# Kernel optimization log

Hardware: AMD Instinct MI355X
Metric: run time of the kernel (lower is better)

## Reference

```python
import jax, jax.numpy as jnp
import numpy as np

B, S, D, H, T, MAXLEN = 8, 1024, 768, 12, 384, 1024
HD = D // H  # spatial head dim = 64
SCALE = HD ** -0.5


def setup_inputs() -> dict:
    key = jax.random.key(0)
    ks = jax.random.split(key, 16)

    def lin(k, din, dout):
        kw, _ = jax.random.split(k)
        w = jax.random.normal(kw, (din, dout), jnp.float32) / np.sqrt(din).astype(np.float32)
        b = jnp.zeros((dout,), jnp.float32)
        return w, b

    Wqs, bqs = lin(ks[0], D, D)
    Wks, bks = lin(ks[1], D, D)
    Wvs, bvs = lin(ks[2], D, D)
    Wqt, bqt = lin(ks[3], T, D)
    Wkt, bkt = lin(ks[4], T, D)
    Wvt, bvt = lin(ks[5], T, D)
    Er = jax.random.normal(ks[6], (MAXLEN, HD), jnp.float32)
    patches = jax.random.normal(ks[7], (B, S, D), jnp.float32)
    time_emb = jax.random.normal(ks[8], (B, T), jnp.float32)
    return dict(patches=patches, time_emb=time_emb,
                Wqs=Wqs, bqs=bqs, Wks=Wks, bks=bks, Wvs=Wvs, bvs=bvs,
                Wqt=Wqt, bqt=bqt, Wkt=Wkt, bkt=bkt, Wvt=Wvt, bvt=bvt, Er=Er)


def _skew(QEr):
    # QEr: [B, H, S, S] -> pad one zero col on the left, reshape, drop first row.
    b, h, r, c = QEr.shape
    padded = jnp.pad(QEr, ((0, 0), (0, 0), (0, 0), (1, 0)))  # [B,H,r,c+1]
    reshaped = padded.reshape(b, h, c + 1, r)
    return reshaped[:, :, 1:, :]  # [B,H,S,S]


def reference(patches, time_emb, Wqs, bqs, Wks, bks, Wvs, bvs,
              Wqt, bqt, Wkt, bkt, Wvt, bvt, Er):
    b, s, _ = patches.shape

    def heads(x):  # [B,S,D] -> [B,H,S,HD]
        return x.reshape(b, -1, H, HD).transpose(0, 2, 1, 3)

    qs = heads(patches @ Wqs + bqs)
    ks = heads(patches @ Wks + bks)
    vs = heads(patches @ Wvs + bvs)
    qt = heads(time_emb @ Wqt + bqt)  # [B,H,1,HD]
    kt = heads(time_emb @ Wkt + bkt)
    vt = heads(time_emb @ Wvt + bvt)

    q = qs + qt
    k = ks + kt
    v = vs + vt

    Er_slice = Er[MAXLEN - s:, :]                      # [S, HD]
    QEr = jnp.einsum('bhsd,td->bhst', qs, Er_slice)    # [B,H,S,S]
    Srel = _skew(QEr)

    scores = (jnp.einsum('bhqd,bhkd->bhqk', q, k) + Srel) * SCALE
    attn = jax.nn.softmax(scores, axis=-1)
    out = jnp.einsum('bhqk,bhkd->bhqd', attn, v)       # [B,H,S,HD]
    return out.transpose(0, 2, 1, 3).reshape(b, s, H * HD)
```

## Files before the change

### kernel.cpp

```cpp
#include <hip/hip_runtime.h>

typedef __attribute__((ext_vector_type(8))) short short8;
typedef __attribute__((ext_vector_type(4))) float floatx4;

#define CSC 0.1803368801f

__device__ __forceinline__ unsigned short f2b(float f){
  unsigned int u = __builtin_bit_cast(unsigned int, f);
  unsigned int r = (u + 0x7fffu + ((u >> 16) & 1u)) >> 16;
  return (unsigned short)r;
}
__device__ __forceinline__ float b2f(unsigned short h){
  unsigned int u = ((unsigned int)h) << 16;
  return __builtin_bit_cast(float, u);
}
__device__ __forceinline__ floatx4 mfma16(short8 a, short8 b, floatx4 c){
  return __builtin_amdgcn_mfma_f32_16x16x32_bf16(a, b, c, 0, 0, 0);
}
__device__ __forceinline__ void gload_lds16(const unsigned short* g, unsigned short* l){
  __builtin_amdgcn_global_load_lds(
      (const __attribute__((address_space(1))) unsigned int*)g,
      (__attribute__((address_space(3))) unsigned int*)l, 16, 0, 0);
}

__global__ __launch_bounds__(256) void prep_kernel(
    const float* __restrict__ patches, const float* __restrict__ Er,
    const float* __restrict__ temb,
    const float* __restrict__ Wqt, const float* __restrict__ bqt,
    const float* __restrict__ Wkt, const float* __restrict__ bkt,
    const float* __restrict__ Wvt, const float* __restrict__ bvt,
    const float* __restrict__ Wqs, const float* __restrict__ Wks,
    const float* __restrict__ Wvs,
    unsigned short* __restrict__ Pb, unsigned short* __restrict__ Erb,
    float* __restrict__ Tmat, unsigned short* __restrict__ Wb){
  int blk = blockIdx.x, tid = threadIdx.x;
  if (blk < 3104){
    const float* src; unsigned short* dst; int idx;
    if (blk < 3072){ idx = blk*2048 + tid*8; src = patches; dst = Pb; }
    else           { idx = (blk-3072)*2048 + tid*8; src = Er; dst = Erb; }
    float4 f0 = *(const float4*)(src + idx);
    float4 f1 = *(const float4*)(src + idx + 4);
    uint4 pk;
    pk.x = (unsigned)f2b(f0.x) | ((unsigned)f2b(f0.y)<<16);
    pk.y = (unsigned)f2b(f0.z) | ((unsigned)f2b(f0.w)<<16);
    pk.z = (unsigned)f2b(f1.x) | ((unsigned)f2b(f1.y)<<16);
    pk.w = (unsigned)f2b(f1.z) | ((unsigned)f2b(f1.w)<<16);
    *(uint4*)(dst + idx) = pk;
  } else if (blk < 3248){
    int idx = blk - 3104;
    int g = idx / 48, rem = idx % 48, bb = rem / 6, kc = rem % 6;
    const float* Wt = (g==0)? Wqt : (g==1)? Wkt : Wvt;
    const float* bt = (g==0)? bqt : (g==1)? bkt : bvt;
    __shared__ float emb[64];
    if (tid < 64) emb[tid] = temb[bb*384 + kc*64 + tid];
    __syncthreads();
    float a0 = 0.f, a1 = 0.f, a2 = 0.f;
    #pragma unroll 8
    for (int t=0;t<64;t++){
      float e = emb[t];
      const float* wr = Wt + (kc*64 + t)*768;
      a0 += e*wr[tid]; a1 += e*wr[tid+256]; a2 += e*wr[tid+512];
    }
    if (kc == 0){ a0 += bt[tid]; a1 += bt[tid+256]; a2 += bt[tid+512]; }
    float s = (g==0) ? CSC : 1.0f;
    float* dst = Tmat + g*6144 + bb*768;
    atomicAdd(&dst[tid],     a0*s);
    atomicAdd(&dst[tid+256], a1*s);
    atomicAdd(&dst[tid+512], a2*s);
  } else {
    int tb = blk - 3248;
    int g = tb / 144, rem = tb % 144;
    int by = rem / 12, bx = rem % 12;
    __shared__ float tile[64][65];
    const float* W = (g==0) ? Wqs : (g==1) ? Wks : Wvs;
    int r0 = by*64, c0 = bx*64;
    int tx = tid & 63, ty = tid >> 6;
    #pragma unroll
    for (int i=0;i<16;i++){
      int r = i*4 + ty;
      tile[r][tx] = W[(r0+r)*768 + c0 + tx];
    }
    __syncthreads();
    unsigned short* dst = Wb + g*589824;
    #pragma unroll
    for (int i=0;i<16;i++){
      int rr = i*4 + ty;
      dst[(c0+rr)*768 + r0 + tx] = f2b(tile[tx][rr]);
    }
  }
}

__global__ __launch_bounds__(256, 3) void qkv_gemm(
    const unsigned short* __restrict__ Pb, const unsigned short* __restrict__ Wb,
    const float* __restrict__ bq, const float* __restrict__ bk,
    const float* __restrict__ bv, const float* __restrict__ Tmat,
    unsigned short* __restrict__ Qs, unsigned short* __restrict__ K,
    unsigned short* __restrict__ V){
  __shared__ unsigned short smem_q[26112];
  unsigned short* a_lds = smem_q;
  unsigned short* b_lds = smem_q + 8192;
  int g = blockIdx.z;
  int m0 = blockIdx.x*128, n0 = blockIdx.y*192;
  int tid = threadIdx.x, w = tid>>6, lane = tid&63, quad = lane>>4, l16 = lane&15;
  int wr = w>>1, wc = w&1;
  const unsigned short* Wg = Wb + g*589824;
  const float* bias = (g==0)? bq : (g==1)? bk : bv;
  floatx4 acc[4][6];
  #pragma unroll
  for (int i=0;i<4;i++)
    #pragma unroll
    for (int j=0;j<6;j++) acc[i][j] = (floatx4){0.f,0.f,0.f,0.f};

  int rsub = lane>>3;
  int csw  = (((lane&7) ^ rsub) << 3);
  int sw   = l16 & 7;

  for (int kt=0; kt<12; kt++){
    int k0 = kt*64;
    __syncthreads();
    #pragma unroll
    for (int j=0;j<4;j++){
      int chunk = w*4 + j;
      int r = chunk*8 + rsub;
      gload_lds16(&Pb[(m0+r)*768 + k0 + csw], &a_lds[chunk*512]);
    }
    #pragma unroll
    for (int j=0;j<6;j++){
      int chunk = w*6 + j;
      int r = chunk*8 + rsub;
      gload_lds16(&Wg[(n0+r)*768 + k0 + csw], &b_lds[chunk*512]);
    }
    __syncthreads();
    #pragma unroll
    for (int ks=0; ks<2; ks++){
      short8 af[4], bf[6];
      int cc = ((ks*4 + quad) ^ sw) << 3;
      #pragma unroll
      for (int mb=0;mb<4;mb++)
        af[mb] = *(const short8*)&a_lds[(wr*64+mb*16+l16)*64 + cc];
      #pragma unroll
      for (int nb=0;nb<6;nb++)
        bf[nb] = *(const short8*)&b_lds[(wc*96+nb*16+l16)*64 + cc];
      #pragma unroll
      for (int mb=0;mb<4;mb++)
        #pragma unroll
        for (int nb=0;nb<6;nb++)
          acc[mb][nb] = mfma16(af[mb], bf[nb], acc[mb][nb]);
    }
  }
  if (g < 2){
    #pragma unroll
    for (int mb=0;mb<4;mb++)
    #pragma unroll
    for (int nb=0;nb<6;nb++)
    #pragma unroll
    for (int reg=0;reg<4;reg++){
      int m = m0 + wr*64 + mb*16 + quad*4 + reg;
      int n = n0 + wc*96 + nb*16 + l16;
      int bb = m >> 10, s = m & 1023, h = n >> 6, hd = n & 63;
      float v = acc[mb][nb][reg] + bias[n];
      int base = (bb*12 + h) << 16;
      if (g == 0){
        Qs[base + (s<<6) + hd] = f2b(v * CSC);
      } else {
        float tadd = Tmat[6144 + bb*768 + n];
        K[base + (s<<6) + hd] = f2b(v + tadd);
      }
    }
  } else {
    __syncthreads();
    int bb = m0 >> 10;
    #pragma unroll
    for (int mb=0;mb<4;mb++)
    #pragma unroll
    for (int nb=0;nb<6;nb++)
    #pragma unroll
    for (int reg=0;reg<4;reg++){
      int ml = wr*64 + mb*16 + quad*4 + reg;
      int nl = wc*96 + nb*16 + l16;
      int n = n0 + nl;
      float v = acc[mb][nb][reg] + bias[n] + Tmat[12288 + bb*768 + n];
      smem_q[nl*136 + ml] = f2b(v);
    }
    __syncthreads();
    int s0 = m0 & 1023;
    #pragma unroll
    for (int i=0;i<12;i++){
      int idx = i*256 + tid;
      int r = idx >> 4, c8 = (idx & 15) << 3;
      int n = n0 + r, h = n >> 6, hd = n & 63;
      int base = (bb*12 + h) << 16;
      *(uint4*)&V[base + (hd<<10) + s0 + c8] = *(const uint4*)&smem_q[r*136 + c8];
    }
  }
}

__global__ __launch_bounds__(256, 3) void attn_kernel(
    const unsigned short* __restrict__ Qsp, const unsigned short* __restrict__ Kp,
    const unsigned short* __restrict__ Vtp, const unsigned short* __restrict__ Erb,
    const float* __restrict__ Tq, float* __restrict__ out){
  __shared__ __align__(16) char smem[29696];
  unsigned short* k_lds  = (unsigned short*)smem;
  unsigned short* v_lds  = (unsigned short*)(smem + 9216);
  unsigned short* pw_all = (unsigned short*)(smem + 18432);

  int tid = threadIdx.x, w = tid>>6, lane = tid&63, quad = lane>>4, l16 = lane&15;
  unsigned short* pw = pw_all + w*1408;
  int wg = blockIdx.x;
  int b = wg & 7, slot = wg >> 3;
  int h = slot >> 3, q0 = (slot & 7) << 7;
  int hb = (b*12 + h) << 16;
  const unsigned short* Qsh = Qsp + hb;
  const unsigned short* Kh  = Kp  + hb;
  const unsigned short* Vh  = Vtp + hb;
  const float* tqv = Tq + b*768 + h*64;

  int frow = w*16 + l16;
  short8 qf[2][2], qlo[2][2], qhi[2][2];
  #pragma unroll
  for (int sub=0; sub<2; sub++){
    int qrow = q0 + sub*64 + frow;
    int qrow1 = (qrow < 1023) ? qrow+1 : 1023;
    #pragma unroll
    for (int ks=0; ks<2; ks++){
      int c = ks*32 + quad*8;
      qlo[sub][ks] = *(const short8*)&Qsh[(qrow <<6) + c];
      qhi[sub][ks] = *(const short8*)&Qsh[(qrow1<<6) + c];
      float4 t0 = *(const float4*)&tqv[c];
      float4 t1 = *(const float4*)&tqv[c+4];
      short8 qq;
      qq[0]=(short)f2b(b2f((unsigned short)qlo[sub][ks][0])+t0.x);
      qq[1]=(short)f2b(b2f((unsigned short)qlo[sub][ks][1])+t0.y);
      qq[2]=(short)f2b(b2f((unsigned short)qlo[sub][ks][2])+t0.z);
      qq[3]=(short)f2b(b2f((unsigned short)qlo[sub][ks][3])+t0.w);
      qq[4]=(short)f2b(b2f((unsigned short)qlo[sub][ks][4])+t1.x);
      qq[5]=(short)f2b(b2f((unsigned short)qlo[sub][ks][5])+t1.y);
      qq[6]=(short)f2b(b2f((unsigned short)qlo[sub][ks][6])+t1.z);
      qq[7]=(short)f2b(b2f((unsigned short)qlo[sub][ks][7])+t1.w);
      qf[sub][ks] = qq;
    }
  }

  float lpart[2][4] = {{0.f,0.f,0.f,0.f},{0.f,0.f,0.f,0.f}};
  floatx4 o_acc[2][4];
  #pragma unroll
  for (int sub=0;sub<2;sub++)
    #pragma unroll
    for (int ob=0;ob<4;ob++) o_acc[sub][ob] = (floatx4){0.f,0.f,0.f,0.f};

  int ql = quad*4;
  int ub_lo = 3 - w;

  int sr = tid>>3, scc = (tid&7)<<3;
  uint4 kr0, kr1, vr0, vr1;
  kr0 = *(const uint4*)&Kh[(sr<<6) + scc];
  kr1 = *(const uint4*)&Kh[((sr+32)<<6) + scc];
  vr0 = *(const uint4*)&Vh[(sr<<10) + scc];
  vr1 = *(const uint4*)&Vh[((sr+32)<<10) + scc];

  for (int kt=0; kt<16; kt++){
    int k0 = kt*64;
    __syncthreads();
    *(uint4*)&k_lds[sr*72 + scc]      = kr0;
    *(uint4*)&k_lds[(sr+32)*72 + scc] = kr1;
    *(uint4*)&v_lds[sr*72 + scc]      = vr0;
    *(uint4*)&v_lds[(sr+32)*72 + scc] = vr1;
    __syncthreads();
    int k0n = (kt < 15) ? k0 + 64 : k0;
    kr0 = *(const uint4*)&Kh[((k0n+sr)<<6) + scc];
    kr1 = *(const uint4*)&Kh[((k0n+sr+32)<<6) + scc];
    vr0 = *(const uint4*)&Vh[(sr<<10) + k0n + scc];
    vr1 = *(const uint4*)&Vh[((sr+32)<<10) + k0n + scc];

    floatx4 sc[2][4];
    __builtin_amdgcn_s_setprio(1);
    #pragma unroll
    for (int nb=0;nb<4;nb++){
      sc[0][nb] = (floatx4){0.f,0.f,0.f,0.f};
      sc[1][nb] = (floatx4){0.f,0.f,0.f,0.f};
      #pragma unroll
      for (int ks=0;ks<2;ks++){
        short8 kf = *(const short8*)&k_lds[(nb*16+l16)*72 + ks*32 + quad*8];
        sc[0][nb] = mfma16(qf[0][ks], kf, sc[0][nb]);
        sc[1][nb] = mfma16(qf[1][ks], kf, sc[1][nb]);
      }
    }
    __builtin_amdgcn_s_setprio(0);

    #pragma unroll
    for (int sub=0; sub<2; sub++){
      int diag = k0 - q0 - sub*64;
      bool needL = (diag <= 0), needU = (diag >= 0);
      bool needSel = (diag == 0) || (diag == 64);
      for (int pass=0; pass<2; pass++){
        if ((pass==0 && !needL) || (pass==1 && !needU)) continue;
        int tbase = (pass==0) ? (960 + diag) : (diag - 65);
        const short8* af = (pass==0) ? qlo[sub] : qhi[sub];
        #pragma unroll
        for (int lb=0; lb<5; lb++){
          int ub = ub_lo + lb;
          int t = tbase + ub*16 + l16;
          t = (t < 0) ? 0 : (t > 1023 ? 1023 : t);
          floatx4 pa = (floatx4){0.f,0.f,0.f,0.f};
          #pragma unroll
          for (int ks=0;ks<2;ks++){
            short8 ef = *(const short8*)&Erb[(t<<6) + ks*32 + quad*8];
            pa = mfma16(af[ks], ef, pa);
          }
          #pragma unroll
          for (int reg=0;reg<4;reg++)
            pw[(ql + reg)*88 + lb*16 + l16] = f2b(pa[reg]);
        }
        #pragma unroll
        for (int nb=0;nb<4;nb++)
        #pragma unroll
        for (int reg=0;reg<4;reg++){
          int qlr = ql + reg;
          int ki = nb*16 + l16;
          float bv = b2f(pw[qlr*88 + 15 + ki - qlr]);
          if (needSel){
            int kq = diag + ki - (w*16 + qlr);
            bool sel = (pass==0) ? (kq <= 0) : (kq >= 2);
            bv = sel ? bv : 0.f;
          }
          sc[sub][nb][reg] += bv;
        }
      }
      #pragma unroll
      for (int nb=0;nb<4;nb++)
      #pragma unroll
      for (int reg=0;reg<4;reg++){
        float p = __builtin_amdgcn_exp2f(sc[sub][nb][reg]);
        lpart[sub][reg] += p;
        pw[(ql + reg)*88 + nb*16 + l16] = f2b(p);
      }
      short8 pf[2];
      #pragma unroll
      for (int ks=0;ks<2;ks++)
        pf[ks] = *(const short8*)&pw[l16*88 + ks*32 + quad*8];
      __builtin_amdgcn_s_setprio(1);
      #pragma unroll
      for (int ob=0;ob<4;ob++){
        #pragma unroll
        for (int ks=0;ks<2;ks++){
          short8 vf = *(const short8*)&v_lds[(ob*16+l16)*72 + ks*32 + quad*8];
          o_acc[sub][ob] = mfma16(pf[ks], vf, o_acc[sub][ob]);
        }
      }
      __builtin_amdgcn_s_setprio(0);
    }
  }
  #pragma unroll
  for (int sub=0;sub<2;sub++){
    float rl[4];
    #pragma unroll
    for (int reg=0;reg<4;reg++){
      float l = lpart[sub][reg];
      #pragma unroll
      for (int off=1; off<16; off<<=1) l += __shfl_xor(l, off);
      rl[reg] = __builtin_amdgcn_rcpf(l);
    }
    #pragma unroll
    for (int ob=0;ob<4;ob++)
    #pragma unroll
    for (int reg=0;reg<4;reg++){
      int s = q0 + sub*64 + w*16 + quad*4 + reg;
      out[((b<<10) + s)*768 + (h<<6) + ob*16 + l16] = o_acc[sub][ob][reg] * rl[reg];
    }
  }
}

extern "C" void kernel_launch(void* const* d_in, const int* in_sizes, int n_in,
                              void* d_out, int out_size, void* d_ws, size_t ws_size,
                              hipStream_t stream) {
  const float* patches  = (const float*)d_in[0];
  const float* time_emb = (const float*)d_in[1];
  const float* Wqs = (const float*)d_in[2];  const float* bqs = (const float*)d_in[3];
  const float* Wks = (const float*)d_in[4];  const float* bks = (const float*)d_in[5];
  const float* Wvs = (const float*)d_in[6];  const float* bvs = (const float*)d_in[7];
  const float* Wqt = (const float*)d_in[8];  const float* bqt = (const float*)d_in[9];
  const float* Wkt = (const float*)d_in[10]; const float* bkt = (const float*)d_in[11];
  const float* Wvt = (const float*)d_in[12]; const float* bvt = (const float*)d_in[13];
  const float* Er  = (const float*)d_in[14];

  unsigned short* Qsp  = (unsigned short*)d_ws;
  unsigned short* Kp   = Qsp + 6291456;
  unsigned short* Vp   = Kp  + 6291456;
  unsigned short* Wbp  = Vp  + 6291456;
  unsigned short* Erbp = Wbp + 1769472;
  unsigned short* Pbp  = Erbp + 65536;
  float*          Tmat = (float*)(Pbp + 6291456);

  float* out = (float*)d_out;

  hipMemsetAsync(Tmat, 0, 3*8*768*sizeof(float), stream);
  hipLaunchKernelGGL(prep_kernel, dim3(3680), dim3(256), 0, stream,
                     patches, Er, time_emb, Wqt, bqt, Wkt, bkt, Wvt, bvt,
                     Wqs, Wks, Wvs, Pbp, Erbp, Tmat, Wbp);
  hipLaunchKernelGGL(qkv_gemm, dim3(64,4,3), dim3(256), 0, stream,
                     Pbp, Wbp, bqs, bks, bvs, Tmat, Qsp, Kp, Vp);
  hipLaunchKernelGGL(attn_kernel, dim3(768), dim3(256), 0, stream,
                     Qsp, Kp, Vp, Erbp, Tmat, out);
}
```

Measured before the change: 305.9 us.

## Split attention key range across two workgroups with atomic accumulation and merge

Each attention workgroup now processes half of the key range, doubling the grid, and accumulates unnormalized outputs and row sums into global buffers via atomicAdd. A separate merge kernel divides by the summed denominators. Launch bounds are raised to allow more resident workgroups. This adds memsets of the output and denominator buffers, float atomics on the full output, and an extra pass over the output.

```diff
diff --git a/kernel.cpp b/kernel.cpp
--- a/kernel.cpp
+++ b/kernel.cpp
@@ -195,10 +195,11 @@
   }
 }
 
-__global__ __launch_bounds__(256, 3) void attn_kernel(
+__global__ __launch_bounds__(256, 4) void attn_kernel(
     const unsigned short* __restrict__ Qsp, const unsigned short* __restrict__ Kp,
     const unsigned short* __restrict__ Vtp, const unsigned short* __restrict__ Erb,
-    const float* __restrict__ Tq, float* __restrict__ out){
+    const float* __restrict__ Tq, float* __restrict__ Oacc,
+    float* __restrict__ Lacc){
   __shared__ __align__(16) char smem[29696];
   unsigned short* k_lds  = (unsigned short*)smem;
   unsigned short* v_lds  = (unsigned short*)(smem + 9216);
@@ -208,7 +209,9 @@
   unsigned short* pw = pw_all + w*1408;
   int wg = blockIdx.x;
   int b = wg & 7, slot = wg >> 3;
-  int h = slot >> 3, q0 = (slot & 7) << 7;
+  int kho = slot & 1;
+  int q0 = ((slot >> 1) & 7) << 7;
+  int h = slot >> 4;
   int hb = (b*12 + h) << 16;
   const unsigned short* Qsh = Qsp + hb;
   const unsigned short* Kh  = Kp  + hb;
@@ -252,13 +255,14 @@
   int ub_lo = 3 - w;
 
   int sr = tid>>3, scc = (tid&7)<<3;
+  int k0i = kho << 9;
   uint4 kr0, kr1, vr0, vr1;
-  kr0 = *(const uint4*)&Kh[(sr<<6) + scc];
-  kr1 = *(const uint4*)&Kh[((sr+32)<<6) + scc];
-  vr0 = *(const uint4*)&Vh[(sr<<10) + scc];
-  vr1 = *(const uint4*)&Vh[((sr+32)<<10) + scc];
-
-  for (int kt=0; kt<16; kt++){
+  kr0 = *(const uint4*)&Kh[((k0i+sr)<<6) + scc];
+  kr1 = *(const uint4*)&Kh[((k0i+sr+32)<<6) + scc];
+  vr0 = *(const uint4*)&Vh[(sr<<10) + k0i + scc];
+  vr1 = *(const uint4*)&Vh[((sr+32)<<10) + k0i + scc];
+
+  for (int kt=kho*8; kt<kho*8+8; kt++){
     int k0 = kt*64;
     __syncthreads();
     *(uint4*)&k_lds[sr*72 + scc]      = kr0;
@@ -352,22 +356,45 @@
   }
   #pragma unroll
   for (int sub=0;sub<2;sub++){
-    float rl[4];
+    float rsum[4];
     #pragma unroll
     for (int reg=0;reg<4;reg++){
       float l = lpart[sub][reg];
       #pragma unroll
       for (int off=1; off<16; off<<=1) l += __shfl_xor(l, off);
-      rl[reg] = __builtin_amdgcn_rcpf(l);
+      rsum[reg] = l;
+    }
+    if (l16 == 0){
+      #pragma unroll
+      for (int reg=0;reg<4;reg++){
+        int s = q0 + sub*64 + w*16 + quad*4 + reg;
+        atomicAdd(&Lacc[(b*12 + h)*1024 + s], rsum[reg]);
+      }
     }
     #pragma unroll
     for (int ob=0;ob<4;ob++)
     #pragma unroll
     for (int reg=0;reg<4;reg++){
       int s = q0 + sub*64 + w*16 + quad*4 + reg;
-      out[((b<<10) + s)*768 + (h<<6) + ob*16 + l16] = o_acc[sub][ob][reg] * rl[reg];
-    }
-  }
+      atomicAdd(&Oacc[((b<<10) + s)*768 + (h<<6) + ob*16 + l16],
+                o_acc[sub][ob][reg]);
+    }
+  }
+}
+
+__global__ __launch_bounds__(256) void attn_merge(
+    float* __restrict__ out, const float* __restrict__ Lacc){
+  int i = blockIdx.x*256 + threadIdx.x;
+  int elem = i << 2;
+  int row = elem / 768;
+  int col = elem - row*768;
+  int hh = col >> 6;
+  int b = row >> 10, s = row & 1023;
+  float l = Lacc[(b*12 + hh)*1024 + s];
+  float r = __builtin_amdgcn_rcpf(l);
+  float4 o = *(const float4*)(out + elem);
+  float4 res = {o.x*r, o.y*r, o.z*r, o.w*r};
+  *(float4*)(out + elem) = res;
 }
 
 extern "C" void kernel_launch(void* const* d_in, const int* in_sizes, int n_in,
@@ -390,6 +417,7 @@
   unsigned short* Erbp = Wbp + 1769472;
   unsigned short* Pbp  = Erbp + 65536;
   float*          Tmat = (float*)(Pbp + 6291456);
+  float*          Lacc = (float*)Pbp;
 
   float* out = (float*)d_out;
 
@@ -399,6 +427,10 @@
                      Wqs, Wks, Wvs, Pbp, Erbp, Tmat, Wbp);
   hipLaunchKernelGGL(qkv_gemm, dim3(64,4,3), dim3(256), 0, stream,
                      Pbp, Wbp, bqs, bks, bvs, Tmat, Qsp, Kp, Vp);
-  hipLaunchKernelGGL(attn_kernel, dim3(768), dim3(256), 0, stream,
-                     Qsp, Kp, Vp, Erbp, Tmat, out);
-}
+  hipMemsetAsync(Lacc, 0, 8*12*1024*sizeof(float), stream);
+  hipMemsetAsync(out,  0, 8*1024*768*sizeof(float), stream);
+  hipLaunchKernelGGL(attn_kernel, dim3(1536), dim3(256), 0, stream,
+                     Qsp, Kp, Vp, Erbp, Tmat, out, Lacc);
+  hipLaunchKernelGGL(attn_merge, dim3(6144), dim3(256), 0, stream,
+                     out, Lacc);
+}
```

Result: slower. 483.1 us (+57.9%).
